# Optimization experiments

Measured on AMD Instinct MI355X. Metric: run time of the kernel, lower is better.

Reference implementation:

```python
import jax, jax.numpy as jnp
import numpy as np


def setup_inputs() -> dict:
    key = jax.random.key(0)
    k1, k2, k3, k4, k5 = jax.random.split(key, 5)
    N_IN, N_OUT = 200000, 400000
    K, P = 27, 50000  # kernel volume (3^3), pairs per kernel offset
    CIN, COUT = 64, 32
    feats = jax.random.normal(k1, (N_IN, CIN), dtype=jnp.float32)
    weight = jax.random.normal(k2, (K, CIN, COUT), dtype=jnp.float32) * (1.0 / np.sqrt(CIN * K))
    bias = jax.random.normal(k3, (COUT,), dtype=jnp.float32) * 0.01
    in_idx = jax.random.randint(k4, (K, P), 0, N_IN, dtype=jnp.int32)
    out_idx = jax.random.randint(k5, (K, P), 0, N_OUT, dtype=jnp.int32)
    return {"feats": feats, "weight": weight, "bias": bias,
            "in_idx": in_idx, "out_idx": out_idx, "n_out": N_OUT}


def reference(feats, weight, bias, in_idx, out_idx, n_out):
    # Rulebook-driven sparse inverse conv3d: gather -> per-offset GEMM -> scatter-add.
    K, P = in_idx.shape
    cout = weight.shape[-1]
    gathered = feats[in_idx]                               # [K, P, Cin]
    contrib = jnp.einsum('kpc,kco->kpo', gathered, weight)  # [K, P, Cout]
    out = jnp.zeros((n_out, cout), dtype=feats.dtype)
    out = out.at[out_idx.reshape(-1)].add(contrib.reshape(-1, cout))
    return out + bias
```

## Files before the change

### kernel.cpp

```cpp
#include <hip/hip_runtime.h>

#define CIN 64
#define COUT 32

typedef __attribute__((ext_vector_type(8))) short bf16x8;
typedef __attribute__((ext_vector_type(4))) float f32x4;

__device__ inline ushort f2bf(float x) {
    union { float f; unsigned u; } v; v.f = x;
    unsigned r = v.u + 0x7fff + ((v.u >> 16) & 1);
    return (ushort)(r >> 16);
}

__global__ __launch_bounds__(256) void zero16_kernel(uint4* __restrict__ p, int n16)
{
    int i = blockIdx.x * blockDim.x + threadIdx.x;
    if (i < n16) p[i] = uint4{0u, 0u, 0u, 0u};
}

__global__ __launch_bounds__(256) void mfma_scatter_pk_kernel(
    const float* __restrict__ feats,
    const float* __restrict__ weight,
    const int* __restrict__ in_idx,
    const int* __restrict__ out_idx,
    ushort* __restrict__ outh,
    int P, int ntiles, int waves_per_k)
{
    const int k    = blockIdx.y;
    const int lane = threadIdx.x & 63;
    const int wav  = blockIdx.x * (blockDim.x >> 6) + (threadIdx.x >> 6);
    const int col  = lane & 15;
    const int kch  = lane >> 4;

    bf16x8 bfrag[2][2];
    const float* __restrict__ Wk = weight + (long)k * CIN * COUT;
    #pragma unroll
    for (int ks = 0; ks < 2; ++ks)
        #pragma unroll
        for (int h = 0; h < 2; ++h) {
            bf16x8 t;
            #pragma unroll
            for (int e = 0; e < 8; ++e)
                t[e] = (short)f2bf(Wk[(ks * 32 + kch * 8 + e) * COUT + 2 * col + h]);
            bfrag[ks][h] = t;
        }

    const int base = k * P;
    for (int tile = wav; tile < ntiles; tile += waves_per_k) {
        const int p0 = tile << 4;
        const int pA = min(p0 + col, P - 1);

        const int row   = in_idx[base + pA];
        const int my_o  = out_idx[base + pA];

        const float* __restrict__ ar = feats + (long)row * CIN + kch * 8;
        float4 f0 = *reinterpret_cast<const float4*>(ar);
        float4 f1 = *reinterpret_cast<const float4*>(ar + 4);
        float4 f2 = *reinterpret_cast<const float4*>(ar + 32);
        float4 f3 = *reinterpret_cast<const float4*>(ar + 36);

        bf16x8 a0, a1;
        a0[0] = (short)f2bf(f0.x); a0[1] = (short)f2bf(f0.y);
        a0[2] = (short)f2bf(f0.z); a0[3] = (short)f2bf(f0.w);
        a0[4] = (short)f2bf(f1.x); a0[5] = (short)f2bf(f1.y);
        a0[6] = (short)f2bf(f1.z); a0[7] = (short)f2bf(f1.w);
        a1[0] = (short)f2bf(f2.x); a1[1] = (short)f2bf(f2.y);
        a1[2] = (short)f2bf(f2.z); a1[3] = (short)f2bf(f2.w);
        a1[4] = (short)f2bf(f3.x); a1[5] = (short)f2bf(f3.y);
        a1[6] = (short)f2bf(f3.z); a1[7] = (short)f2bf(f3.w);

        f32x4 acc0 = {0.f, 0.f, 0.f, 0.f};
        f32x4 acc1 = {0.f, 0.f, 0.f, 0.f};
        acc0 = __builtin_amdgcn_mfma_f32_16x16x32_bf16(a0, bfrag[0][0], acc0, 0, 0, 0);
        acc0 = __builtin_amdgcn_mfma_f32_16x16x32_bf16(a1, bfrag[1][0], acc0, 0, 0, 0);
        acc1 = __builtin_amdgcn_mfma_f32_16x16x32_bf16(a0, bfrag[0][1], acc1, 0, 0, 0);
        acc1 = __builtin_amdgcn_mfma_f32_16x16x32_bf16(a1, bfrag[1][1], acc1, 0, 0, 0);

        #pragma unroll
        for (int r = 0; r < 4; ++r) {
            const int prow = p0 + kch * 4 + r;
            const int orow = __shfl(my_o, kch * 4 + r, 64);
            if (prow < P) {
                union { _Float16 h[2]; unsigned u; } pk;
                pk.h[0] = (_Float16)acc0[r];
                pk.h[1] = (_Float16)acc1[r];
                const ushort* dst = outh + (long)orow * COUT + 2 * col;
                asm volatile("global_atomic_pk_add_f16 %0, %1, off"
                             :: "v"((unsigned long long)dst), "v"(pk.u)
                             : "memory");
            }
        }
    }
}

__global__ __launch_bounds__(256) void finalize_kernel(
    const unsigned* __restrict__ outh_u, const float* __restrict__ bias,
    float* __restrict__ out, int n4)
{
    int i = blockIdx.x * blockDim.x + threadIdx.x;
    if (i < n4) {
        unsigned u0 = outh_u[2 * i], u1 = outh_u[2 * i + 1];
        int ch = (i * 4) & (COUT - 1);
        union { unsigned u; _Float16 h[2]; } a, b;
        a.u = u0; b.u = u1;
        float4 o;
        o.x = (float)a.h[0] + bias[ch + 0];
        o.y = (float)a.h[1] + bias[ch + 1];
        o.z = (float)b.h[0] + bias[ch + 2];
        o.w = (float)b.h[1] + bias[ch + 3];
        reinterpret_cast<float4*>(out)[i] = o;
    }
}


__global__ __launch_bounds__(256) void bias_init_kernel(
    float* __restrict__ out, const float* __restrict__ bias, int total)
{
    int i = (blockIdx.x * blockDim.x + threadIdx.x) * 4;
    if (i < total) {
        int ch = i & (COUT - 1);
        float4 b;
        b.x = bias[ch + 0]; b.y = bias[ch + 1];
        b.z = bias[ch + 2]; b.w = bias[ch + 3];
        *reinterpret_cast<float4*>(out + i) = b;
    }
}

__global__ __launch_bounds__(256) void scatter_gemm_kernel(
    const float* __restrict__ feats,
    const float* __restrict__ weight,
    const int* __restrict__ in_idx,
    const int* __restrict__ out_idx,
    float* __restrict__ out,
    int P, int n_groups)
{
    const int k        = blockIdx.y;
    const int lane     = threadIdx.x & 31;
    const int group_id = blockIdx.x * (blockDim.x >> 5) + (threadIdx.x >> 5);

    float w[CIN];
    const float* __restrict__ Wk = weight + (long)k * CIN * COUT;
    #pragma unroll
    for (int c = 0; c < CIN; ++c) w[c] = Wk[c * COUT + lane];

    const int base    = k * P;
    const int nchunks = (P + 31) >> 5;
    for (int ch = group_id; ch < nchunks; ch += n_groups) {
        const int p0 = ch << 5;
        const int n  = min(32, P - p0);
        int my_in = 0, my_out = 0;
        if (lane < n) {
            my_in  = in_idx[base + p0 + lane];
            my_out = out_idx[base + p0 + lane];
        }
        #pragma unroll 4
        for (int j = 0; j < n; ++j) {
            const int in = __shfl(my_in,  j, 32);
            const int o  = __shfl(my_out, j, 32);
            const float4* __restrict__ fr =
                reinterpret_cast<const float4*>(feats + (long)in * CIN);
            float acc = 0.0f;
            #pragma unroll
            for (int c4 = 0; c4 < CIN / 4; ++c4) {
                float4 f = fr[c4];
                acc += f.x * w[4 * c4 + 0];
                acc += f.y * w[4 * c4 + 1];
                acc += f.z * w[4 * c4 + 2];
                acc += f.w * w[4 * c4 + 3];
            }
            atomicAdd(out + (long)o * COUT + lane, acc);
        }
    }
}


extern "C" void kernel_launch(void* const* d_in, const int* in_sizes, int n_in,
                              void* d_out, int out_size, void* d_ws, size_t ws_size,
                              hipStream_t stream) {
    const float* feats   = (const float*)d_in[0];
    const float* weight  = (const float*)d_in[1];
    const float* bias    = (const float*)d_in[2];
    const int*   in_idx  = (const int*)d_in[3];
    const int*   out_idx = (const int*)d_in[4];
    float*       out     = (float*)d_out;

    const int K = in_sizes[1] / (CIN * COUT);
    const int P = in_sizes[3] / K;

    size_t need = (size_t)out_size * 2;

    if (need > ws_size || (out_size & 7) != 0) {
        int total4 = out_size / 4;
        bias_init_kernel<<<(total4 + 255) / 256, 256, 0, stream>>>(out, bias, out_size);
        const int blocks_x = 96;
        const int n_groups = blocks_x * (256 / 32);
        dim3 grid(blocks_x, K);
        scatter_gemm_kernel<<<grid, 256, 0, stream>>>(feats, weight, in_idx, out_idx,
                                                      out, P, n_groups);
        return;
    }

    ushort* outh = (ushort*)d_ws;

    {
        int n16 = (out_size * 2) / 16;
        zero16_kernel<<<(n16 + 255) / 256, 256, 0, stream>>>((uint4*)outh, n16);
    }

    {
        const int ntiles      = (P + 15) / 16;
        const int blocks_x    = 196;
        const int waves_per_k = blocks_x * 4;
        dim3 grid(blocks_x, K);
        mfma_scatter_pk_kernel<<<grid, 256, 0, stream>>>(feats, weight, in_idx,
                                                         out_idx, outh, P, ntiles,
                                                         waves_per_k);
    }

    finalize_kernel<<<(out_size / 4 + 255) / 256, 256, 0, stream>>>(
        (const unsigned*)outh, bias, out, out_size / 4);
}
```

Baseline: 104.2 us.

## Software-prefetch next tile's gather and use builtin packed half atomic add

```diff
diff --git a/kernel.cpp b/kernel.cpp
--- a/kernel.cpp
+++ b/kernel.cpp
@@ -1,4 +1,5 @@
 #include <hip/hip_runtime.h>
+#include <hip/hip_fp16.h>
 
 #define CIN 64
 #define COUT 32
@@ -46,28 +47,45 @@
         }
 
     const int base = k * P;
-    for (int tile = wav; tile < ntiles; tile += waves_per_k) {
-        const int p0 = tile << 4;
-        const int pA = min(p0 + col, P - 1);
-
-        const int row   = in_idx[base + pA];
-        const int my_o  = out_idx[base + pA];
-
-        const float* __restrict__ ar = feats + (long)row * CIN + kch * 8;
-        float4 f0 = *reinterpret_cast<const float4*>(ar);
-        float4 f1 = *reinterpret_cast<const float4*>(ar + 4);
-        float4 f2 = *reinterpret_cast<const float4*>(ar + 32);
-        float4 f3 = *reinterpret_cast<const float4*>(ar + 36);
+
+    int tile = wav;
+    if (tile >= ntiles) return;
+
+    int pA  = min((tile << 4) + col, P - 1);
+    int row = in_idx[base + pA];
+    int oidx = out_idx[base + pA];
+    const float* ar = feats + (long)row * CIN + kch * 8;
+    float4 f0 = *reinterpret_cast<const float4*>(ar);
+    float4 f1 = *reinterpret_cast<const float4*>(ar + 4);
+    float4 f2 = *reinterpret_cast<const float4*>(ar + 32);
+    float4 f3 = *reinterpret_cast<const float4*>(ar + 36);
+
+    while (tile < ntiles) {
+        const int p0    = tile << 4;
+        const int my_o  = oidx;
+        float4 c0 = f0, c1 = f1, c2 = f2, c3 = f3;
+
+        const int next = tile + waves_per_k;
+        if (next < ntiles) {
+            pA   = min((next << 4) + col, P - 1);
+            row  = in_idx[base + pA];
+            oidx = out_idx[base + pA];
+            ar = feats + (long)row * CIN + kch * 8;
+            f0 = *reinterpret_cast<const float4*>(ar);
+            f1 = *reinterpret_cast<const float4*>(ar + 4);
+            f2 = *reinterpret_cast<const float4*>(ar + 32);
+            f3 = *reinterpret_cast<const float4*>(ar + 36);
+        }
 
         bf16x8 a0, a1;
-        a0[0] = (short)f2bf(f0.x); a0[1] = (short)f2bf(f0.y);
-        a0[2] = (short)f2bf(f0.z); a0[3] = (short)f2bf(f0.w);
-        a0[4] = (short)f2bf(f1.x); a0[5] = (short)f2bf(f1.y);
-        a0[6] = (short)f2bf(f1.z); a0[7] = (short)f2bf(f1.w);
-        a1[0] = (short)f2bf(f2.x); a1[1] = (short)f2bf(f2.y);
-        a1[2] = (short)f2bf(f2.z); a1[3] = (short)f2bf(f2.w);
-        a1[4] = (short)f2bf(f3.x); a1[5] = (short)f2bf(f3.y);
-        a1[6] = (short)f2bf(f3.z); a1[7] = (short)f2bf(f3.w);
+        a0[0] = (short)f2bf(c0.x); a0[1] = (short)f2bf(c0.y);
+        a0[2] = (short)f2bf(c0.z); a0[3] = (short)f2bf(c0.w);
+        a0[4] = (short)f2bf(c1.x); a0[5] = (short)f2bf(c1.y);
+        a0[6] = (short)f2bf(c1.z); a0[7] = (short)f2bf(c1.w);
+        a1[0] = (short)f2bf(c2.x); a1[1] = (short)f2bf(c2.y);
+        a1[2] = (short)f2bf(c2.z); a1[3] = (short)f2bf(c2.w);
+        a1[4] = (short)f2bf(c3.x); a1[5] = (short)f2bf(c3.y);
+        a1[6] = (short)f2bf(c3.z); a1[7] = (short)f2bf(c3.w);
 
         f32x4 acc0 = {0.f, 0.f, 0.f, 0.f};
         f32x4 acc1 = {0.f, 0.f, 0.f, 0.f};
@@ -81,15 +99,13 @@
             const int prow = p0 + kch * 4 + r;
             const int orow = __shfl(my_o, kch * 4 + r, 64);
             if (prow < P) {
-                union { _Float16 h[2]; unsigned u; } pk;
-                pk.h[0] = (_Float16)acc0[r];
-                pk.h[1] = (_Float16)acc1[r];
-                const ushort* dst = outh + (long)orow * COUT + 2 * col;
-                asm volatile("global_atomic_pk_add_f16 %0, %1, off"
-                             :: "v"((unsigned long long)dst), "v"(pk.u)
-                             : "memory");
+                __half2 v = __floats2half2_rn(acc0[r], acc1[r]);
+                __half2* dst = reinterpret_cast<__half2*>(
+                    outh + (long)orow * COUT + 2 * col);
+                unsafeAtomicAdd(dst, v);
             }
         }
+        tile = next;
     }
 }
 
```

New measurement: 104.2 us. No clear change (+0.0%).
